# Kernel tuning notes

Hardware: AMD Instinct MI355X
Metric: run time of the kernel (lower is better)

## Reference

```python
import jax, jax.numpy as jnp
import numpy as np

N = 50000      # entity nodes
E = 300000     # edges in edge_index_all (and edge_index)
E_LINE = 50000 # line-graph edges over relations
EH = 128       # e_hidden
RH = 64        # r_hidden
REL1 = 2000
REL2 = 2000
GH = 3 * EH + RH  # GAT hidden = 448


def seg_softmax(e, idx, n):
    # torch_geometric softmax: exp(e - segmax[idx]) / (segsum + 1e-16)
    m = jax.ops.segment_max(e, idx, num_segments=n)
    ex = jnp.exp(e - m[idx])
    s = jax.ops.segment_sum(ex, idx, num_segments=n)
    return ex / (s[idx] + 1e-16)


def setup_inputs() -> dict:
    key = jax.random.key(0)
    ks = jax.random.split(key, 24)

    def nrm(k, shape, s=0.1):
        return jax.random.normal(k, shape, dtype=jnp.float32) * s

    # edges without self loops: dst = (src + off) % N, off in [1, N)
    src = jax.random.randint(ks[0], (E,), 0, N)
    off = jax.random.randint(ks[1], (E,), 1, N)
    edge_index_all = jnp.stack([src, (src + off) % N])
    src2 = jax.random.randint(ks[2], (E,), 0, N)
    off2 = jax.random.randint(ks[3], (E,), 1, N)
    edge_index = jnp.stack([src2, (src2 + off2) % N])

    rel = jax.random.randint(ks[4], (E,), 0, REL1)
    rel_all = jax.random.randint(ks[5], (E,), 0, 2 * REL1)
    line_graph_index_out = jax.random.randint(ks[6], (2, E_LINE), 0, REL1)
    line_graph_index_in = jax.random.randint(ks[7], (2, E_LINE), 0, REL1)

    return {
        "x_e": nrm(ks[8], (N, EH), 1.0),
        "rel_emb1": nrm(ks[9], (REL1, RH), 1.0),
        "rel_emb2": nrm(ks[10], (REL2, RH), 1.0),
        "w_gcn1": nrm(ks[11], (EH, EH)),
        "Wh1": nrm(ks[12], (EH, EH)),
        "bh1": nrm(ks[13], (EH,)),
        "w_gcn2": nrm(ks[14], (EH, EH)),
        "Wh2": nrm(ks[15], (EH, EH)),
        "bh2": nrm(ks[16], (EH,)),
        "ai_l": nrm(ks[17], (RH,)),
        "aj_l": nrm(ks[18], (RH,)),
        "w_tw": nrm(ks[19], (2 * EH + RH,)),
        "ai_g": nrm(ks[20], (GH,)),
        "aj_g": nrm(ks[21], (GH,)),
        "ar_g": nrm(ks[22], (RH,)),
        "edge_index": edge_index,
        "rel": rel,
        "edge_index_all": edge_index_all,
        "rel_all": rel_all,
        "line_graph_index_out": line_graph_index_out,
        "line_graph_index_in": line_graph_index_in,
    }


def mrea_forward(x_e, rel_emb1, w_gcn1, Wh1, bh1, w_gcn2, Wh2, bh2,
                 ai_l, aj_l, w_tw, ai_g, aj_g, ar_g,
                 edge_index_all, rel_all, lg_out, lg_in):
    n = x_e.shape[0]
    # GCN/GAT unpack: edge_index_j, edge_index_i = edge_index (row0=j, row1=i)
    j, i = edge_index_all[0], edge_index_all[1]

    def gcn(x, W):
        deg = jax.ops.segment_sum(jnp.ones(i.shape, x.dtype), i, num_segments=n)
        dinv = jnp.where(deg > 0, deg ** -0.5, 0.0)
        norm = dinv[j] * dinv[i]  # [E]
        agg = jax.nn.relu(jax.ops.segment_sum(norm[:, None] * x[j], i, num_segments=n))
        return agg @ W.T

    def highway(x1, x2, W, b):
        g = jax.nn.sigmoid(x1 @ W.T + b)
        return g * x2 + (1.0 - g) * x1

    x = highway(x_e, gcn(x_e, w_gcn1), Wh1, bh1)
    x = highway(x, gcn(x, w_gcn2), Wh2, bh2)

    # L_GAT over relation line graphs (softmax grouped by edge_index_j, as in source)
    nr = rel_emb1.shape[0]
    def l_gat(xr, ei):
        jj, ii = ei[0], ei[1]
        e = (xr @ ai_l)[ii] + (xr @ aj_l)[jj]
        alpha = seg_softmax(jax.nn.leaky_relu(e), jj, nr)
        return jax.nn.relu(jax.ops.segment_sum(alpha[:, None] * xr[jj], ii, num_segments=nr))

    rel_emb = jnp.concatenate([l_gat(rel_emb1, lg_out), l_gat(rel_emb1, lg_in)], axis=0)  # [2*REL1, RH]

    # T-wise attention: edge_index_i, edge_index_j = edge_index_all (row0=i, row1=j)
    ti, tj = edge_index_all[0], edge_index_all[1]
    feat = jnp.concatenate([x[ti], rel_emb[rel_all], x[tj]], axis=1)  # [E, 2e+r]
    att = seg_softmax(feat @ w_tw, ti, n)
    x_agg = jax.nn.relu(jax.ops.segment_sum(feat * att[:, None], ti, num_segments=n))
    x_rel = jnp.concatenate([x, x_agg], axis=1)  # [N, 3e+r]

    # GAT on x_rel with relation bias (row0=j, row1=i)
    e = (x_rel @ ai_g)[i] + (x_rel @ aj_g)[j] + (rel_emb @ ar_g)[rel_all]
    alpha = seg_softmax(jax.nn.leaky_relu(e), i, n)
    gat_out = jax.nn.relu(jax.ops.segment_sum(alpha[:, None] * x_rel[j], i, num_segments=n))

    return jnp.concatenate([x_rel, gat_out], axis=1)  # [N, 2*(3e+r)]


def reference(x_e, rel_emb1, rel_emb2, w_gcn1, Wh1, bh1, w_gcn2, Wh2, bh2,
              ai_l, aj_l, w_tw, ai_g, aj_g, ar_g,
              edge_index, rel, edge_index_all, rel_all,
              line_graph_index_out, line_graph_index_in):
    # Branch rel.max()+1 == rel1_size is true for our data -> rel_emb1 used.
    # rel_emb2, edge_index, rel do not enter the computation on this branch.
    return mrea_forward(x_e, rel_emb1, w_gcn1, Wh1, bh1, w_gcn2, Wh2, bh2,
                        ai_l, aj_l, w_tw, ai_g, aj_g, ar_g,
                        edge_index_all, rel_all,
                        line_graph_index_out, line_graph_index_in)
```

## Files before the change

### kernel.cpp

```cpp
#include <hip/hip_runtime.h>
#include <math.h>

#define NN 50000
#define EE 300000
#define EL 50000
#define EH 128
#define RH 64
#define R1 2000
#define NR2 4000
#define OD 896
#define NT64 782
#define GCNB 12500
#define CAP 32
#define LGCAP 64

using f32x4 = __attribute__((ext_vector_type(4))) float;
using bf16x8 = __attribute__((ext_vector_type(8))) short;

__device__ __forceinline__ float leaky(float x) { return x >= 0.f ? x : 0.01f * x; }

__device__ __forceinline__ void atomicMaxF(float* addr, float val) {
    if (val >= 0.f) atomicMax((int*)addr, __float_as_int(val));
    else            atomicMin((unsigned int*)addr, __float_as_uint(val));
}

__device__ __forceinline__ short bfrn(float f) {
    unsigned u = __float_as_uint(f);
    return (short)((u + 0x7FFFu + ((u >> 16) & 1u)) >> 16);
}
__device__ __forceinline__ void cvt1(float f, short& h, short& l) {
    h = bfrn(f);
    float hf = __uint_as_float(((unsigned)(unsigned short)h) << 16);
    l = bfrn(f - hf);
}
__device__ __forceinline__ void cvt8(float4 a, float4 b, bf16x8& hi, bf16x8& lo) {
    float v[8] = {a.x, a.y, a.z, a.w, b.x, b.y, b.z, b.w};
#pragma unroll
    for (int e = 0; e < 8; ++e) {
        short h, l;
        cvt1(v[e], h, l);
        hi[e] = h;
        lo[e] = l;
    }
}

__device__ __forceinline__ float2 bf2f(unsigned u) {
    float2 f;
    f.x = __uint_as_float(u << 16);
    f.y = __uint_as_float(u & 0xFFFF0000u);
    return f;
}

__global__ __launch_bounds__(256) void k_sij(const float* __restrict__ rel1,
                                             const float* __restrict__ ai_l, const float* __restrict__ aj_l,
                                             float* __restrict__ s_i, float* __restrict__ s_j) {
    int r = blockIdx.x * 256 + threadIdx.x;
    if (r < R1) {
        const float* m = rel1 + (long)r * 64;
        float a = 0.f, bb = 0.f;
#pragma unroll
        for (int c = 0; c < 64; ++c) {
            float v = m[c];
            a += v * ai_l[c];
            bb += v * aj_l[c];
        }
        s_i[r] = a;
        s_j[r] = bb;
    }
}

__global__ void k_fill_all(const int* __restrict__ e0, const int* __restrict__ e1,
                           const int* __restrict__ rel_all,
                           int* __restrict__ cnt0, int* __restrict__ cnt1,
                           int2* __restrict__ csr0p, int2* __restrict__ csr1p,
                           const int* __restrict__ lgo, const int* __restrict__ lgi,
                           const float* __restrict__ s_i, const float* __restrict__ s_j,
                           float* __restrict__ lgsc, float* __restrict__ lgmax,
                           int* __restrict__ lgcnt, int* __restrict__ lgsrc,
                           int* __restrict__ lgpos,
                           const float* __restrict__ W0, const float* __restrict__ W1,
                           const float* __restrict__ W2, const float* __restrict__ W3,
                           float* __restrict__ P0, float* __restrict__ P1,
                           float* __restrict__ P2, float* __restrict__ P3) {
    if (blockIdx.x < 32) {
        int slot = blockIdx.x * 256 + threadIdx.x;
        int m = slot >> 11;
        int rem = slot & 2047;
        int kb = rem >> 9;
        int nt = (rem >> 6) & 7;
        int l = rem & 63;
        const float* W = m == 0 ? W0 : m == 1 ? W1 : m == 2 ? W2 : W3;
        float* P = m == 0 ? P0 : m == 1 ? P1 : m == 2 ? P2 : P3;
        int n = (nt << 4) + (l & 15);
        int k0 = (kb << 5) + ((l >> 4) << 2);
        float4 a0 = *(const float4*)(W + (n << 7) + k0);
        float4 a1 = *(const float4*)(W + (n << 7) + k0 + 16);
        bf16x8 hv, lv;
        cvt8(a0, a1, hv, lv);
        int u = ((kb << 3) + nt) * 64 + l;
        *(bf16x8*)(P + ((long)u << 2)) = hv;
        *(bf16x8*)(P + 8192 + ((long)u << 2)) = lv;
        return;
    }
    int gid = (blockIdx.x - 32) * blockDim.x + threadIdx.x;
    int stride = (gridDim.x - 32) * blockDim.x;
    for (int i = gid; i < EE; i += stride) {
        int j0 = e0[i], i1 = e1[i], ra = rel_all[i];
        int p = atomicAdd(&cnt0[j0], 1);
        if (p < CAP) csr0p[(j0 << 5) + p] = make_int2(i1, ra);
        int q = atomicAdd(&cnt1[i1], 1);
        if (q < CAP) csr1p[(i1 << 5) + q] = make_int2(j0, ra);
    }
    for (int e = gid; e < 2 * EL; e += stride) {
        int g1 = e >= EL;
        int ee = g1 ? e - EL : e;
        const int* L = g1 ? lgi : lgo;
        int jj = L[ee], ii = L[ee + EL];
        float v = leaky(s_j[jj] + s_i[ii]);
        lgsc[e] = v;
        atomicMaxF(&lgmax[(g1 ? R1 : 0) + jj], v);
        int g = (g1 ? R1 : 0) + ii;
        int p = atomicAdd(&lgcnt[g], 1);
        if (p < LGCAP) {
            lgsrc[(g << 6) + p] = jj;
            lgpos[e] = (g << 6) + p;
        } else {
            lgpos[e] = -1;
        }
    }
}

template <bool RELU>
__device__ __forceinline__ void mfma_phase(const float* __restrict__ A, const float* __restrict__ P,
                                           float4* lds4, int tid, int l, int arow, f32x4 (&acc)[8]) {
#pragma unroll
    for (int s = 0; s < 2; ++s) {
        const float* Ap = A + ((long)arow << 7) + (s << 6) + ((l >> 4) << 2);
        float4 a0 = *(const float4*)(Ap);
        float4 a1 = *(const float4*)(Ap + 16);
        float4 a2 = *(const float4*)(Ap + 32);
        float4 a3 = *(const float4*)(Ap + 48);
        if (RELU) {
            a0.x = fmaxf(a0.x, 0.f); a0.y = fmaxf(a0.y, 0.f); a0.z = fmaxf(a0.z, 0.f); a0.w = fmaxf(a0.w, 0.f);
            a1.x = fmaxf(a1.x, 0.f); a1.y = fmaxf(a1.y, 0.f); a1.z = fmaxf(a1.z, 0.f); a1.w = fmaxf(a1.w, 0.f);
            a2.x = fmaxf(a2.x, 0.f); a2.y = fmaxf(a2.y, 0.f); a2.z = fmaxf(a2.z, 0.f); a2.w = fmaxf(a2.w, 0.f);
            a3.x = fmaxf(a3.x, 0.f); a3.y = fmaxf(a3.y, 0.f); a3.z = fmaxf(a3.z, 0.f); a3.w = fmaxf(a3.w, 0.f);
        }
        __syncthreads();
        const float4* srcH = (const float4*)P + (s << 10);
        const float4* srcL = (const float4*)P + 2048 + (s << 10);
#pragma unroll
        for (int i = 0; i < 4; ++i) {
            lds4[(i << 8) + tid] = srcH[(i << 8) + tid];
            lds4[1024 + (i << 8) + tid] = srcL[(i << 8) + tid];
        }
        __syncthreads();
        bf16x8 ah0, al0, ah1, al1;
        cvt8(a0, a1, ah0, al0);
        cvt8(a2, a3, ah1, al1);
        const bf16x8* BH = (const bf16x8*)lds4;
        const bf16x8* BL = BH + 1024;
#pragma unroll
        for (int nt = 0; nt < 8; ++nt) {
            bf16x8 bh0 = BH[(nt << 6) + l];
            bf16x8 bl0 = BL[(nt << 6) + l];
            bf16x8 bh1 = BH[512 + (nt << 6) + l];
            bf16x8 bl1 = BL[512 + (nt << 6) + l];
            f32x4 c = acc[nt];
            c = __builtin_amdgcn_mfma_f32_16x16x32_bf16(ah0, bh0, c, 0, 0, 0);
            c = __builtin_amdgcn_mfma_f32_16x16x32_bf16(al0, bh0, c, 0, 0, 0);
            c = __builtin_amdgcn_mfma_f32_16x16x32_bf16(ah0, bl0, c, 0, 0, 0);
            c = __builtin_amdgcn_mfma_f32_16x16x32_bf16(ah1, bh1, c, 0, 0, 0);
            c = __builtin_amdgcn_mfma_f32_16x16x32_bf16(al1, bh1, c, 0, 0, 0);
            c = __builtin_amdgcn_mfma_f32_16x16x32_bf16(ah1, bl1, c, 0, 0, 0);
            acc[nt] = c;
        }
    }
}

template <bool XB>
__global__ __launch_bounds__(256) void k_gcn_mfma(const float* __restrict__ Agg, const float* __restrict__ Xin,
                                                  float* __restrict__ Xout,
                                                  const float* __restrict__ Pg, const float* __restrict__ Ph,
                                                  const float* __restrict__ b,
                                                  const float* __restrict__ wtw192, float* __restrict__ xb,
                                                  unsigned short* __restrict__ xm) {
    __shared__ float4 lds4[2048];
    const int tid = threadIdx.x;
    const int l = tid & 63;
    const int wv = tid >> 6;
    const int l15 = l & 15;
    const int l4 = l >> 4;
    const int rowbase = blockIdx.x * 64 + (wv << 4);
    int arow = rowbase + l15;
    if (arow >= NN) arow = NN - 1;
    f32x4 tAcc[8], hAcc[8];
#pragma unroll
    for (int nt = 0; nt < 8; ++nt) {
        tAcc[nt] = {0.f, 0.f, 0.f, 0.f};
        hAcc[nt] = {0.f, 0.f, 0.f, 0.f};
    }
    mfma_phase<true>(Agg, Pg, lds4, tid, l, arow, tAcc);
    mfma_phase<false>(Xin, Ph, lds4, tid, l, arow, hAcc);
    const int r0 = rowbase + (l4 << 2);
    float xbp[4] = {0.f, 0.f, 0.f, 0.f};
#pragma unroll
    for (int nt = 0; nt < 8; ++nt) {
        float bv = b[(nt << 4) + l15];
#pragma unroll
        for (int r = 0; r < 4; ++r) {
            int row = r0 + r;
            if (row < NN) {
                long off = ((long)row << 7) + (nt << 4) + l15;
                float xv = Xin[off];
                float g = 1.f / (1.f + expf(-(hAcc[nt][r] + bv)));
                float ov = g * tAcc[nt][r] + (1.f - g) * xv;
                Xout[off] = ov;
                if (XB) {
                    xbp[r] += ov * wtw192[(nt << 4) + l15];
                    xm[off] = (unsigned short)bfrn(ov);
                }
            }
        }
    }
    if (XB) {
#pragma unroll
        for (int r = 0; r < 4; ++r) {
#pragma unroll
            for (int off = 1; off < 16; off <<= 1) xbp[r] += __shfl_xor(xbp[r], off);
            int row = r0 + r;
            if (l15 == 0 && row < NN) xb[row] = xbp[r];
        }
    }
}

template <int MODE>
__global__ __launch_bounds__(256) void k_gcn_gather(const int2* __restrict__ csr1p, const int* __restrict__ cnt1,
                                                    const float* __restrict__ x, float* __restrict__ agg,
                                                    const int* __restrict__ lgo, const int* __restrict__ lgi,
                                                    const float* __restrict__ lgsc, const float* __restrict__ lgmax,
                                                    float* __restrict__ lgsum,
                                                    const int* __restrict__ lgpos, float* __restrict__ lgscp,
                                                    const int* __restrict__ lgcnt, const int* __restrict__ lgsrc,
                                                    const float* __restrict__ rel1, float* __restrict__ relemb,
                                                    const float* __restrict__ wtw, const float* __restrict__ arg,
                                                    float* __restrict__ rw, float* __restrict__ gr) {
    if (blockIdx.x < GCNB) {
        int w = blockIdx.x * 4 + (threadIdx.x >> 6);
        int lane = threadIdx.x & 63;
        int cw = cnt1[w];
        int deg = cw > CAP ? CAP : cw;
        int b = w << 5;
        float dd = cw > 0 ? rsqrtf((float)cw) : 0.f;
        int sidx = 0;
        float wt = 0.f;
        if (lane < deg) {
            sidx = csr1p[b + lane].x;
            int cs = cnt1[sidx];
            wt = dd * (cs > 0 ? rsqrtf((float)cs) : 0.f);
        }
        const float2* x2 = (const float2*)x;
        float2 aA = {0.f, 0.f}, aB = {0.f, 0.f}, aC = {0.f, 0.f}, aD = {0.f, 0.f};
        int j = 0;
        for (; j + 3 < deg; j += 4) {
            int s0 = __shfl(sidx, j), s1 = __shfl(sidx, j + 1);
            int s2 = __shfl(sidx, j + 2), s3 = __shfl(sidx, j + 3);
            float w0 = __shfl(wt, j), w1 = __shfl(wt, j + 1);
            float w2 = __shfl(wt, j + 2), w3 = __shfl(wt, j + 3);
            float2 v0 = x2[((long)s0 << 6) + lane];
            float2 v1 = x2[((long)s1 << 6) + lane];
            float2 v2 = x2[((long)s2 << 6) + lane];
            float2 v3 = x2[((long)s3 << 6) + lane];
            aA.x += w0 * v0.x; aA.y += w0 * v0.y;
            aB.x += w1 * v1.x; aB.y += w1 * v1.y;
            aC.x += w2 * v2.x; aC.y += w2 * v2.y;
            aD.x += w3 * v3.x; aD.y += w3 * v3.y;
        }
        for (; j < deg; ++j) {
            int s0 = __shfl(sidx, j);
            float w0 = __shfl(wt, j);
            float2 v0 = x2[((long)s0 << 6) + lane];
            aA.x += w0 * v0.x; aA.y += w0 * v0.y;
        }
        float2 r;
        r.x = (aA.x + aB.x) + (aC.x + aD.x);
        r.y = (aA.y + aB.y) + (aC.y + aD.y);
        ((float2*)agg)[((long)w << 6) + lane] = r;
        return;
    }
    if (MODE == 1) {
        int gid = (blockIdx.x - GCNB) * 256 + threadIdx.x;
        const int stride = 391 * 256;
        for (int e = gid; e < 2 * EL; e += stride) {
            int g1 = e >= EL;
            int ee = g1 ? e - EL : e;
            const int* L = g1 ? lgi : lgo;
            int jjg = (g1 ? R1 : 0) + L[ee];
            float ex = expf(lgsc[e] - lgmax[jjg]);
            int lp = lgpos[e];
            if (lp >= 0) lgscp[lp] = ex;
            atomicAdd(&lgsum[jjg], ex);
        }
    } else {
        int d = (blockIdx.x - GCNB) * 4 + (threadIdx.x >> 6);
        int lane = threadIdx.x & 63;
        if (d >= NR2) return;
        int base = d >= R1 ? R1 : 0;
        int cd = lgcnt[d];
        int deg = cd > LGCAP ? LGCAP : cd;
        int b = d << 6;
        int src = 0;
        float al = 0.f;
        if (lane < deg) {
            src = lgsrc[b + lane];
            al = lgscp[b + lane] / (lgsum[base + src] + 1e-16f);
        }
        float aA = 0.f, aB = 0.f;
        int j = 0;
        for (; j + 1 < deg; j += 2) {
            float a0 = __shfl(al, j), a1 = __shfl(al, j + 1);
            int s0 = __shfl(src, j), s1 = __shfl(src, j + 1);
            aA += a0 * rel1[((long)s0 << 6) + lane];
            aB += a1 * rel1[((long)s1 << 6) + lane];
        }
        if (j < deg) {
            float a0 = __shfl(al, j);
            int s0 = __shfl(src, j);
            aA += a0 * rel1[((long)s0 << 6) + lane];
        }
        float v = fmaxf(aA + aB, 0.f);
        relemb[((long)d << 6) + lane] = v;
        float pa = v * wtw[128 + lane];
        float pb = v * arg[lane];
        for (int off = 32; off > 0; off >>= 1) {
            pa += __shfl_down(pa, off);
            pb += __shfl_down(pb, off);
        }
        if (lane == 0) { rw[d] = pa; gr[d] = pb; }
    }
}

__global__ __launch_bounds__(256) void k_tw_gather(const int2* __restrict__ csr0p, const int* __restrict__ cnt0,
                                                   const float* __restrict__ xb, const float* __restrict__ rw,
                                                   const float* __restrict__ x, const unsigned short* __restrict__ xm,
                                                   const float* __restrict__ relemb,
                                                   const float* __restrict__ aig, const float* __restrict__ ajg,
                                                   float* __restrict__ out,
                                                   float* __restrict__ ga, float* __restrict__ gb) {
    int w = (blockIdx.x * blockDim.x + threadIdx.x) >> 6;
    int lane = threadIdx.x & 63;
    if (w >= NN) return;
    int cw = cnt0[w];
    int deg = cw > CAP ? CAP : cw;
    int b = w << 5;
    int trx = 0, trr = 0;
    float v = -INFINITY;
    if (lane < deg) {
        int2 tr = csr0p[b + lane];
        trx = tr.x; trr = tr.y;
        v = xb[trx] + rw[trr];
    }
    float m = v;
#pragma unroll
    for (int off = 32; off > 0; off >>= 1) m = fmaxf(m, __shfl_xor(m, off));
    float al = (lane < deg) ? expf(v - m) : 0.f;
    float sum = al;
#pragma unroll
    for (int off = 32; off > 0; off >>= 1) sum += __shfl_xor(sum, off);
    const float2* x2 = (const float2*)x;
    int c2 = 2 * lane;
    float2 xt = x2[((long)w << 6) + lane];
    float a2A = 0.f, a2B = 0.f;
    float2 a3A = {0.f, 0.f}, a3B = {0.f, 0.f};
    int j = 0;
    for (; j + 1 < deg; j += 2) {
        float alA = __shfl(al, j), alB = __shfl(al, j + 1);
        int xA = __shfl(trx, j), xB = __shfl(trx, j + 1);
        int yA = __shfl(trr, j), yB = __shfl(trr, j + 1);
        a2A += alA * relemb[((long)yA << 6) + lane];
        a2B += alB * relemb[((long)yB << 6) + lane];
        unsigned uA = *(const unsigned*)(xm + ((long)xA << 7) + c2);
        unsigned uB = *(const unsigned*)(xm + ((long)xB << 7) + c2);
        float2 xvA = bf2f(uA);
        float2 xvB = bf2f(uB);
        a3A.x += alA * xvA.x; a3A.y += alA * xvA.y;
        a3B.x += alB * xvB.x; a3B.y += alB * xvB.y;
    }
    if (j < deg) {
        float alA = __shfl(al, j);
        int xA = __shfl(trx, j);
        int yA = __shfl(trr, j);
        a2A += alA * relemb[((long)yA << 6) + lane];
        float2 xvA = bf2f(*(const unsigned*)(xm + ((long)xA << 7) + c2));
        a3A.x += alA * xvA.x; a3A.y += alA * xvA.y;
    }
    float r = 1.f / (sum + 1e-16f);
    float sr = sum * r;
    float2 v23;
    v23.x = fmaxf(xt.x * sr, 0.f);
    v23.y = fmaxf(xt.y * sr, 0.f);
    float v4 = fmaxf((a2A + a2B) * r, 0.f);
    float2 v56;
    v56.x = fmaxf((a3A.x + a3B.x) * r, 0.f);
    v56.y = fmaxf((a3A.y + a3B.y) * r, 0.f);
    float* o = out + (long)w * OD;
    *(float2*)(o + c2) = xt;
    *(float2*)(o + 128 + c2) = v23;
    o[256 + lane] = v4;
    *(float2*)(o + 320 + c2) = v56;
    float da = xt.x * aig[c2] + xt.y * aig[c2 + 1] + v23.x * aig[128 + c2] + v23.y * aig[129 + c2] +
               v4 * aig[256 + lane] + v56.x * aig[320 + c2] + v56.y * aig[321 + c2];
    float db = xt.x * ajg[c2] + xt.y * ajg[c2 + 1] + v23.x * ajg[128 + c2] + v23.y * ajg[129 + c2] +
               v4 * ajg[256 + lane] + v56.x * ajg[320 + c2] + v56.y * ajg[321 + c2];
    for (int off = 32; off > 0; off >>= 1) {
        da += __shfl_down(da, off);
        db += __shfl_down(db, off);
    }
    if (lane == 0) { ga[w] = da; gb[w] = db; }
}

__global__ __launch_bounds__(256) void k_gat_gather(const int2* __restrict__ csr1p, const int* __restrict__ cnt1,
                                                    const float* __restrict__ ga, const float* __restrict__ gb,
                                                    const float* __restrict__ gr,
                                                    const unsigned short* __restrict__ xm,
                                                    float* __restrict__ out) {
    int w = (blockIdx.x * blockDim.x + threadIdx.x) >> 6;
    int lane = threadIdx.x & 63;
    if (w >= NN) return;
    int cw = cnt1[w];
    int deg = cw > CAP ? CAP : cw;
    int b = w << 5;
    float gaw = ga[w];
    int px = 0;
    float v = -INFINITY;
    if (lane < deg) {
        int2 p = csr1p[b + lane];
        px = p.x;
        v = leaky(gaw + gb[px] + gr[p.y]);
    }
    float m = v;
#pragma unroll
    for (int off = 32; off > 0; off >>= 1) m = fmaxf(m, __shfl_xor(m, off));
    float al = (lane < deg) ? expf(v - m) : 0.f;
    float sum = al;
#pragma unroll
    for (int off = 32; off > 0; off >>= 1) sum += __shfl_xor(sum, off);
    int c2 = 2 * lane;
    float2 c0A = {0.f, 0.f}, c0B = {0.f, 0.f};
    float2 c2A = {0.f, 0.f}, c2B = {0.f, 0.f};
    float  c4A = 0.f, c4B = 0.f;
    float2 c5A = {0.f, 0.f}, c5B = {0.f, 0.f};
    int j = 0;
    for (; j + 1 < deg; j += 2) {
        float al0 = __shfl(al, j), al1 = __shfl(al, j + 1);
        int p0 = __shfl(px, j), p1 = __shfl(px, j + 1);
        float2 x0 = bf2f(*(const unsigned*)(xm + ((long)p0 << 7) + c2));
        float2 x1v = bf2f(*(const unsigned*)(xm + ((long)p1 << 7) + c2));
        const float* r0 = out + (long)p0 * OD;
        const float* r1 = out + (long)p1 * OD;
        float  y0 = r0[256 + lane], y1 = r1[256 + lane];
        float2 z0 = *(const float2*)(r0 + 320 + c2);
        float2 z1 = *(const float2*)(r1 + 320 + c2);
        c0A.x += al0 * x0.x + al1 * x1v.x;  c0A.y += al0 * x0.y + al1 * x1v.y;
        c2A.x += al0 * fmaxf(x0.x, 0.f) + al1 * fmaxf(x1v.x, 0.f);
        c2A.y += al0 * fmaxf(x0.y, 0.f) + al1 * fmaxf(x1v.y, 0.f);
        c4A += al0 * y0 + al1 * y1;
        c5A.x += al0 * z0.x + al1 * z1.x;  c5A.y += al0 * z0.y + al1 * z1.y;
    }
    if (j < deg) {
        float al0 = __shfl(al, j);
        int p0 = __shfl(px, j);
        float2 xv = bf2f(*(const unsigned*)(xm + ((long)p0 << 7) + c2));
        const float* row = out + (long)p0 * OD;
        float  yv = row[256 + lane];
        float2 zv = *(const float2*)(row + 320 + c2);
        c0B.x += al0 * xv.x; c0B.y += al0 * xv.y;
        c2B.x += al0 * fmaxf(xv.x, 0.f); c2B.y += al0 * fmaxf(xv.y, 0.f);
        c4B += al0 * yv;
        c5B.x += al0 * zv.x; c5B.y += al0 * zv.y;
    }
    float r = 1.f / (sum + 1e-16f);
    float* o = out + (long)w * OD + 448;
    float2 w0, w2, w5;
    w0.x = fmaxf((c0A.x + c0B.x) * r, 0.f);
    w0.y = fmaxf((c0A.y + c0B.y) * r, 0.f);
    w2.x = fmaxf((c2A.x + c2B.x) * r, 0.f);
    w2.y = fmaxf((c2A.y + c2B.y) * r, 0.f);
    w5.x = fmaxf((c5A.x + c5B.x) * r, 0.f);
    w5.y = fmaxf((c5A.y + c5B.y) * r, 0.f);
    *(float2*)(o + c2) = w0;
    *(float2*)(o + 128 + c2) = w2;
    o[256 + lane] = fmaxf((c4A + c4B) * r, 0.f);
    *(float2*)(o + 320 + c2) = w5;
}

static inline int gs(long n) {
    long b = (n + 255) / 256;
    return (int)(b > 8192 ? 8192 : b);
}

extern "C" void kernel_launch(void* const* d_in, const int* in_sizes, int n_in,
                              void* d_out, int out_size, void* d_ws, size_t ws_size,
                              hipStream_t stream) {
    (void)in_sizes; (void)n_in; (void)out_size; (void)ws_size;

    const float* x_e   = (const float*)d_in[0];
    const float* rel1  = (const float*)d_in[1];
    const float* wgcn1 = (const float*)d_in[3];
    const float* Wh1   = (const float*)d_in[4];
    const float* bh1   = (const float*)d_in[5];
    const float* wgcn2 = (const float*)d_in[6];
    const float* Wh2   = (const float*)d_in[7];
    const float* bh2   = (const float*)d_in[8];
    const float* ai_l  = (const float*)d_in[9];
    const float* aj_l  = (const float*)d_in[10];
    const float* w_tw  = (const float*)d_in[11];
    const float* ai_g  = (const float*)d_in[12];
    const float* aj_g  = (const float*)d_in[13];
    const float* ar_g  = (const float*)d_in[14];
    const int* eia     = (const int*)d_in[17];
    const int* rel_all = (const int*)d_in[18];
    const int* lgo     = (const int*)d_in[19];
    const int* lgi     = (const int*)d_in[20];

    const int* e0 = eia;
    const int* e1 = eia + EE;

    float* out = (float*)d_out;
    float* ws  = (float*)d_ws;

    float* x1     = ws + 0;
    float* agg    = ws + 6400000;
    float* relemb = ws + 12800000;
    float* lgsum  = ws + 13056000;
    int*   cnt0   = (int*)(ws + 13060000);
    int*   cnt1   = (int*)(ws + 13110000);
    int*   lgcnt  = (int*)(ws + 13160000);
    float* lgmax  = ws + 13164000;
    float* xb     = ws + 13218000;
    float* rw     = ws + 13268000;
    float* gr     = ws + 13272000;
    float* ga     = ws + 13276000;
    float* gb     = ws + 13326000;
    int2*  csr0p  = (int2*)(ws + 13376000);
    int2*  csr1p  = (int2*)(ws + 16576000);
    float* wt1    = ws + 19776000;
    float* wt2    = ws + 19792384;
    float* wt3    = ws + 19808768;
    float* wt4    = ws + 19825152;
    float* s_i    = ws + 19841536;
    float* s_j    = ws + 19843536;
    float* lgsc   = ws + 19845536;
    float* lgscp  = ws + 19945536;
    int*   lgsrc  = (int*)(ws + 20201536);
    int*   lgpos  = (int*)(ws + 20457536);
    unsigned short* xm = (unsigned short*)(ws + 20557536);

    hipMemsetAsync(lgsum, 0, (size_t)108000 * sizeof(float), stream);
    hipMemsetAsync(lgmax, 0xFF, (size_t)NR2 * sizeof(float), stream);
    k_sij<<<8, 256, 0, stream>>>(rel1, ai_l, aj_l, s_i, s_j);

    k_fill_all<<<gs(EE) + 32, 256, 0, stream>>>(e0, e1, rel_all, cnt0, cnt1, csr0p, csr1p,
                                                lgo, lgi, s_i, s_j, lgsc, lgmax, lgcnt, lgsrc, lgpos,
                                                wgcn1, Wh1, wgcn2, Wh2, wt1, wt2, wt3, wt4);

    k_gcn_gather<1><<<GCNB + 391, 256, 0, stream>>>(csr1p, cnt1, x_e, agg,
                                                    lgo, lgi, lgsc, lgmax, lgsum,
                                                    lgpos, lgscp, lgcnt, lgsrc, rel1, relemb,
                                                    w_tw, ar_g, rw, gr);
    k_gcn_mfma<false><<<NT64, 256, 0, stream>>>(agg, x_e, x1, wt1, wt2, bh1, nullptr, nullptr, nullptr);

    k_gcn_gather<2><<<GCNB + 1000, 256, 0, stream>>>(csr1p, cnt1, x1, agg,
                                                     lgo, lgi, lgsc, lgmax, lgsum,
                                                     lgpos, lgscp, lgcnt, lgsrc, rel1, relemb,
                                                     w_tw, ar_g, rw, gr);
    k_gcn_mfma<true><<<NT64, 256, 0, stream>>>(agg, x1, x1, wt3, wt4, bh2, w_tw + 192, xb, xm);

    k_tw_gather<<<12500, 256, 0, stream>>>(csr0p, cnt0, xb, rw, x1, xm, relemb, ai_g, aj_g, out, ga, gb);

    k_gat_gather<<<12500, 256, 0, stream>>>(csr1p, cnt1, ga, gb, gr, xm, out);
}
```

Before: 332.9 us.

## Gather GAT neighbor features from compact bf16 copy and unroll gathers by four

k_tw_gather now also writes a compact bf16 copy of the 192 aggregated columns for each node. k_gat_gather reads its per-neighbor features from that copy instead of strided fp32 rows of the output, which cuts gathered bytes per edge. Both gather loops are unrolled to four neighbors per step to keep more loads in flight. The two memsets are merged into one zero-fill that now also initialises lgmax to 0 instead of all-ones bits. The cost is an extra write of the bf16 buffer and bf16 rounding of the gathered GAT inputs, which lowers accuracy.

```diff
diff --git a/kernel.cpp b/kernel.cpp
--- a/kernel.cpp
+++ b/kernel.cpp
@@ -49,6 +49,12 @@
     f.x = __uint_as_float(u << 16);
     f.y = __uint_as_float(u & 0xFFFF0000u);
     return f;
+}
+__device__ __forceinline__ float bf1f(unsigned short u) {
+    return __uint_as_float(((unsigned)u) << 16);
+}
+__device__ __forceinline__ unsigned packbf(float a, float b) {
+    return (unsigned)(unsigned short)bfrn(a) | (((unsigned)(unsigned short)bfrn(b)) << 16);
 }
 
 __global__ __launch_bounds__(256) void k_sij(const float* __restrict__ rel1,
@@ -346,7 +352,8 @@
                                                    const float* __restrict__ relemb,
                                                    const float* __restrict__ aig, const float* __restrict__ ajg,
                                                    float* __restrict__ out,
-                                                   float* __restrict__ ga, float* __restrict__ gb) {
+                                                   float* __restrict__ ga, float* __restrict__ gb,
+                                                   unsigned short* __restrict__ ym) {
     int w = (blockIdx.x * blockDim.x + threadIdx.x) >> 6;
     int lane = threadIdx.x & 63;
     if (w >= NN) return;
@@ -373,20 +380,27 @@
     float a2A = 0.f, a2B = 0.f;
     float2 a3A = {0.f, 0.f}, a3B = {0.f, 0.f};
     int j = 0;
-    for (; j + 1 < deg; j += 2) {
-        float alA = __shfl(al, j), alB = __shfl(al, j + 1);
-        int xA = __shfl(trx, j), xB = __shfl(trx, j + 1);
-        int yA = __shfl(trr, j), yB = __shfl(trr, j + 1);
-        a2A += alA * relemb[((long)yA << 6) + lane];
-        a2B += alB * relemb[((long)yB << 6) + lane];
-        unsigned uA = *(const unsigned*)(xm + ((long)xA << 7) + c2);
-        unsigned uB = *(const unsigned*)(xm + ((long)xB << 7) + c2);
-        float2 xvA = bf2f(uA);
-        float2 xvB = bf2f(uB);
-        a3A.x += alA * xvA.x; a3A.y += alA * xvA.y;
-        a3B.x += alB * xvB.x; a3B.y += alB * xvB.y;
-    }
-    if (j < deg) {
+    for (; j + 3 < deg; j += 4) {
+        float al0 = __shfl(al, j), al1 = __shfl(al, j + 1);
+        float al2 = __shfl(al, j + 2), al3 = __shfl(al, j + 3);
+        int x0i = __shfl(trx, j), x1i = __shfl(trx, j + 1);
+        int x2i = __shfl(trx, j + 2), x3i = __shfl(trx, j + 3);
+        int y0i = __shfl(trr, j), y1i = __shfl(trr, j + 1);
+        int y2i = __shfl(trr, j + 2), y3i = __shfl(trr, j + 3);
+        float r0 = relemb[((long)y0i << 6) + lane];
+        float r1 = relemb[((long)y1i << 6) + lane];
+        float r2 = relemb[((long)y2i << 6) + lane];
+        float r3 = relemb[((long)y3i << 6) + lane];
+        float2 v0 = bf2f(*(const unsigned*)(xm + ((long)x0i << 7) + c2));
+        float2 v1 = bf2f(*(const unsigned*)(xm + ((long)x1i << 7) + c2));
+        float2 v2 = bf2f(*(const unsigned*)(xm + ((long)x2i << 7) + c2));
+        float2 v3 = bf2f(*(const unsigned*)(xm + ((long)x3i << 7) + c2));
+        a2A += al0 * r0 + al1 * r1;
+        a2B += al2 * r2 + al3 * r3;
+        a3A.x += al0 * v0.x + al1 * v1.x;  a3A.y += al0 * v0.y + al1 * v1.y;
+        a3B.x += al2 * v2.x + al3 * v3.x;  a3B.y += al2 * v2.y + al3 * v3.y;
+    }
+    for (; j < deg; ++j) {
         float alA = __shfl(al, j);
         int xA = __shfl(trx, j);
         int yA = __shfl(trr, j);
@@ -408,6 +422,9 @@
     *(float2*)(o + 128 + c2) = v23;
     o[256 + lane] = v4;
     *(float2*)(o + 320 + c2) = v56;
+    unsigned short* yr = ym + (long)w * 192;
+    yr[lane] = (unsigned short)bfrn(v4);
+    *(unsigned*)(yr + 64 + c2) = packbf(v56.x, v56.y);
     float da = xt.x * aig[c2] + xt.y * aig[c2 + 1] + v23.x * aig[128 + c2] + v23.y * aig[129 + c2] +
                v4 * aig[256 + lane] + v56.x * aig[320 + c2] + v56.y * aig[321 + c2];
     float db = xt.x * ajg[c2] + xt.y * ajg[c2 + 1] + v23.x * ajg[128 + c2] + v23.y * ajg[129 + c2] +
@@ -423,6 +440,7 @@
                                                     const float* __restrict__ ga, const float* __restrict__ gb,
                                                     const float* __restrict__ gr,
                                                     const unsigned short* __restrict__ xm,
+                                                    const unsigned short* __restrict__ ym,
                                                     float* __restrict__ out) {
     int w = (blockIdx.x * blockDim.x + threadIdx.x) >> 6;
     int lane = threadIdx.x & 63;
@@ -451,29 +469,43 @@
     float  c4A = 0.f, c4B = 0.f;
     float2 c5A = {0.f, 0.f}, c5B = {0.f, 0.f};
     int j = 0;
-    for (; j + 1 < deg; j += 2) {
+    for (; j + 3 < deg; j += 4) {
         float al0 = __shfl(al, j), al1 = __shfl(al, j + 1);
+        float al2 = __shfl(al, j + 2), al3 = __shfl(al, j + 3);
         int p0 = __shfl(px, j), p1 = __shfl(px, j + 1);
+        int p2 = __shfl(px, j + 2), p3 = __shfl(px, j + 3);
+        const unsigned short* y0 = ym + (long)p0 * 192;
+        const unsigned short* y1 = ym + (long)p1 * 192;
+        const unsigned short* y2 = ym + (long)p2 * 192;
+        const unsigned short* y3 = ym + (long)p3 * 192;
         float2 x0 = bf2f(*(const unsigned*)(xm + ((long)p0 << 7) + c2));
         float2 x1v = bf2f(*(const unsigned*)(xm + ((long)p1 << 7) + c2));
-        const float* r0 = out + (long)p0 * OD;
-        const float* r1 = out + (long)p1 * OD;
-        float  y0 = r0[256 + lane], y1 = r1[256 + lane];
-        float2 z0 = *(const float2*)(r0 + 320 + c2);
-        float2 z1 = *(const float2*)(r1 + 320 + c2);
-        c0A.x += al0 * x0.x + al1 * x1v.x;  c0A.y += al0 * x0.y + al1 * x1v.y;
+        float2 x2v = bf2f(*(const unsigned*)(xm + ((long)p2 << 7) + c2));
+        float2 x3v = bf2f(*(const unsigned*)(xm + ((long)p3 << 7) + c2));
+        float yv0 = bf1f(y0[lane]), yv1 = bf1f(y1[lane]);
+        float yv2 = bf1f(y2[lane]), yv3 = bf1f(y3[lane]);
+        float2 z0 = bf2f(*(const unsigned*)(y0 + 64 + c2));
+        float2 z1 = bf2f(*(const unsigned*)(y1 + 64 + c2));
+        float2 z2 = bf2f(*(const unsigned*)(y2 + 64 + c2));
+        float2 z3 = bf2f(*(const unsigned*)(y3 + 64 + c2));
+        c0A.x += al0 * x0.x + al1 * x1v.x;   c0A.y += al0 * x0.y + al1 * x1v.y;
+        c0B.x += al2 * x2v.x + al3 * x3v.x;  c0B.y += al2 * x2v.y + al3 * x3v.y;
         c2A.x += al0 * fmaxf(x0.x, 0.f) + al1 * fmaxf(x1v.x, 0.f);
         c2A.y += al0 * fmaxf(x0.y, 0.f) + al1 * fmaxf(x1v.y, 0.f);
-        c4A += al0 * y0 + al1 * y1;
+        c2B.x += al2 * fmaxf(x2v.x, 0.f) + al3 * fmaxf(x3v.x, 0.f);
+        c2B.y += al2 * fmaxf(x2v.y, 0.f) + al3 * fmaxf(x3v.y, 0.f);
+        c4A += al0 * yv0 + al1 * yv1;
+        c4B += al2 * yv2 + al3 * yv3;
         c5A.x += al0 * z0.x + al1 * z1.x;  c5A.y += al0 * z0.y + al1 * z1.y;
-    }
-    if (j < deg) {
+        c5B.x += al2 * z2.x + al3 * z3.x;  c5B.y += al2 * z2.y + al3 * z3.y;
+    }
+    for (; j < deg; ++j) {
         float al0 = __shfl(al, j);
         int p0 = __shfl(px, j);
+        const unsigned short* y0 = ym + (long)p0 * 192;
         float2 xv = bf2f(*(const unsigned*)(xm + ((long)p0 << 7) + c2));
-        const float* row = out + (long)p0 * OD;
-        float  yv = row[256 + lane];
-        float2 zv = *(const float2*)(row + 320 + c2);
+        float yv = bf1f(y0[lane]);
+        float2 zv = bf2f(*(const unsigned*)(y0 + 64 + c2));
         c0B.x += al0 * xv.x; c0B.y += al0 * xv.y;
         c2B.x += al0 * fmaxf(xv.x, 0.f); c2B.y += al0 * fmaxf(xv.y, 0.f);
         c4B += al0 * yv;
@@ -555,9 +587,9 @@
     int*   lgsrc  = (int*)(ws + 20201536);
     int*   lgpos  = (int*)(ws + 20457536);
     unsigned short* xm = (unsigned short*)(ws + 20557536);
-
-    hipMemsetAsync(lgsum, 0, (size_t)108000 * sizeof(float), stream);
-    hipMemsetAsync(lgmax, 0xFF, (size_t)NR2 * sizeof(float), stream);
+    unsigned short* ym = (unsigned short*)(ws + 23757536);
+
+    hipMemsetAsync(lgsum, 0, (size_t)112000 * sizeof(float), stream);
     k_sij<<<8, 256, 0, stream>>>(rel1, ai_l, aj_l, s_i, s_j);
 
     k_fill_all<<<gs(EE) + 32, 256, 0, stream>>>(e0, e1, rel_all, cnt0, cnt1, csr0p, csr1p,
@@ -576,7 +608,7 @@
                                                      w_tw, ar_g, rw, gr);
     k_gcn_mfma<true><<<NT64, 256, 0, stream>>>(agg, x1, x1, wt3, wt4, bh2, w_tw + 192, xb, xm);
 
-    k_tw_gather<<<12500, 256, 0, stream>>>(csr0p, cnt0, xb, rw, x1, xm, relemb, ai_g, aj_g, out, ga, gb);
-
-    k_gat_gather<<<12500, 256, 0, stream>>>(csr1p, cnt1, ga, gb, gr, xm, out);
-}
+    k_tw_gather<<<12500, 256, 0, stream>>>(csr0p, cnt0, xb, rw, x1, xm, relemb, ai_g, aj_g, out, ga, gb, ym);
+
+    k_gat_gather<<<12500, 256, 0, stream>>>(csr1p, cnt1, ga, gb, gr, xm, ym, out);
+}
```

After: 317.6 us. 1.05x faster.
